# Kernel optimization log

Hardware: AMD Instinct MI355X
Metric: run time of the kernel (lower is better)

## Reference

```python
import jax, jax.numpy as jnp
import numpy as np

B, T, D, H = 2, 2048, 1024, 16
HD = D // H
FF = 4 * D
EPS = 1e-5


def rmsnorm(x, w):
    var = jnp.mean(jnp.square(x), axis=-1, keepdims=True)
    return x * jax.lax.rsqrt(var + EPS) * w


def setup_inputs() -> dict:
    key = jax.random.key(0)
    ks = jax.random.split(key, 17)
    sc = 0.02
    d = {}
    d["x"] = jax.random.normal(ks[0], (B, T, D), jnp.float32)
    d["x_token"] = jax.random.normal(ks[1], (B, T, D), jnp.float32)
    d["pos_emb"] = jax.random.normal(ks[2], (T, D), jnp.float32)
    d["lc_weight"] = jax.random.normal(ks[3], (1,), jnp.float32)
    d["Wq"] = jax.random.normal(ks[4], (D, D), jnp.float32) * sc  # per-head query weights stacked
    d["Wk"] = jax.random.normal(ks[5], (D, D), jnp.float32) * sc
    d["Wv"] = jax.random.normal(ks[6], (D, D), jnp.float32) * sc
    d["proj_w"] = jax.random.normal(ks[7], (D, D), jnp.float32) * sc
    d["proj_b"] = jnp.zeros((D,), jnp.float32)
    d["w1_w"] = jax.random.normal(ks[8], (FF, D), jnp.float32) * sc
    d["w1_b"] = jnp.zeros((FF,), jnp.float32)
    d["w2_w"] = jax.random.normal(ks[9], (D, FF), jnp.float32) * sc
    d["w2_b"] = jnp.zeros((D,), jnp.float32)
    d["w3_w"] = jax.random.normal(ks[10], (FF, D), jnp.float32) * sc
    d["w3_b"] = jnp.zeros((FF,), jnp.float32)
    d["norm1_w"] = jnp.ones((D,), jnp.float32)
    d["norm2_w"] = jnp.ones((D,), jnp.float32)
    return d


def reference(x, x_token, pos_emb, lc_weight, Wq, Wk, Wv, proj_w, proj_b,
              w1_w, w1_b, w2_w, w2_b, w3_w, w3_b, norm1_w, norm2_w):
    lc = jax.nn.sigmoid(lc_weight)  # scalar gate
    x_att = lc * x + (1.0 - lc) * x_token
    xn = rmsnorm(x_att, norm1_w)

    # q, v from normed gated input; k from raw positional embedding (faithful to source)
    q = (xn @ Wq.T).reshape(B, T, H, HD)
    k = (pos_emb @ Wk.T).reshape(T, H, HD)
    v = (xn @ Wv.T).reshape(B, T, H, HD)

    # NOTE: scale uses full model dim E (=D), not head_size, as in the source
    scores = jnp.einsum('bqhd,khd->bhqk', q, k) * (D ** -0.5)
    causal = jnp.tril(jnp.ones((T, T), bool))
    scores = jnp.where(causal, scores, -jnp.inf)
    p = jax.nn.softmax(scores, axis=-1)
    attn = jnp.einsum('bhqk,bkhd->bqhd', p, v).reshape(B, T, D)

    x = x + attn @ proj_w.T + proj_b

    xn2 = rmsnorm(x, norm2_w)
    h = jax.nn.silu(xn2 @ w1_w.T + w1_b) * (xn2 @ w3_w.T + w3_b)
    return x + h @ w2_w.T + w2_b
```

## Files before the change

kernel.cpp:

```cpp
#include <hip/hip_runtime.h>
#include <hip/hip_bf16.h>


typedef __hip_bfloat16 bf16;
typedef __attribute__((ext_vector_type(8))) short bf16x8;
typedef __attribute__((ext_vector_type(4))) float floatx4;

constexpr int cB = 2, cT = 2048, cD = 1024, cH = 16, cFF = 4096;
constexpr float cEPS = 1e-5f;
constexpr unsigned BF16_ONES = 0x3F803F80u;

__device__ __forceinline__ float b2f(bf16 x) { return __bfloat162float(x); }
__device__ __forceinline__ bf16  f2b(float x) { return __float2bfloat16(x); }
__device__ __forceinline__ unsigned short f2bu(float x) {
  bf16 t = __float2bfloat16(x);
  union { bf16 b; unsigned short u; } cv;
  cv.b = t;
  return cv.u;
}
__device__ __forceinline__ float loadR(const bf16* p)  { return b2f(*p); }
__device__ __forceinline__ float loadR(const float* p) { return *p; }

__device__ __forceinline__ void gload16(const bf16* g, unsigned short* l) {
  __builtin_amdgcn_global_load_lds(
      (const __attribute__((address_space(1))) void*)g,
      (__attribute__((address_space(3))) void*)l, 16, 0, 0);
}

__device__ __forceinline__ int xcd_remap1(int lin, int n) {
  return (lin & 7) * (n >> 3) + (lin >> 3);
}
__device__ __forceinline__ void xcd_remap(int& bx, int& by, int gx, int gy) {
  const int nwg = gx * gy;
  const int lin = by * gx + bx;
  const int nl  = xcd_remap1(lin, nwg);
  bx = nl % gx;
  by = nl / gx;
}

struct ConvArgs {
  const void* src[17];
  bf16* dst[17];
  int n[17];
  int sb[17];
};

__global__ __launch_bounds__(256) void convert_all_k(ConvArgs a) {
  const int bid = blockIdx.x;
  int seg = 0;
#pragma unroll
  for (int i = 1; i < 17; i++) seg = (bid >= a.sb[i]) ? i : seg;
  const int n = a.n[seg];
  const int i0 = (bid - a.sb[seg]) * 2048 + threadIdx.x * 8;
  if (i0 >= n) return;
  const bool isb = (((const unsigned*)a.src[15])[0] == BF16_ONES);
  const void* src = a.src[seg];
  bf16* dst = a.dst[seg];
  if (i0 + 8 <= n) {
    if (isb) {
      *(int4*)(dst + i0) = *(const int4*)((const bf16*)src + i0);
    } else {
      float4 f0 = *(const float4*)((const float*)src + i0);
      float4 f1 = *(const float4*)((const float*)src + i0 + 4);
      int4 ro;
      bf16* po = (bf16*)&ro;
      po[0] = f2b(f0.x); po[1] = f2b(f0.y); po[2] = f2b(f0.z); po[3] = f2b(f0.w);
      po[4] = f2b(f1.x); po[5] = f2b(f1.y); po[6] = f2b(f1.z); po[7] = f2b(f1.w);
      *(int4*)(dst + i0) = ro;
    }
  } else {
    for (int j = i0; j < n; j++)
      dst[j] = isb ? ((const bf16*)src)[j] : f2b(((const float*)src)[j]);
  }
}

template <int OUTK, typename ResT>
__device__ __forceinline__ void gemm_core64(
    const bf16* __restrict__ A, const bf16* __restrict__ W,
    const bf16* __restrict__ bias, const ResT* __restrict__ R,
    void* __restrict__ Cv,
    int N, int Kst, int kb, int klen, int m0, int n0,
    unsigned short* As, unsigned short* Bs)
{
  const int tid  = threadIdx.x;
  const int wave = tid >> 6;
  const int lane = tid & 63;
  const int l15  = lane & 15;
  const int quad = lane >> 4;
  const int wm   = (wave >> 1) * 64;
  const int wn   = (wave & 1) * 32;

  const int lr  = lane >> 2;
  const int lc8 = (lane & 3) * 8;
  const bf16* Ag0 = A + (size_t)(m0 + wave * 32 + lr) * Kst + kb + lc8;
  const bf16* Ag1 = Ag0 + (size_t)16 * Kst;
  const bf16* Bg0 = W + (size_t)(n0 + wave * 16 + lr) * Kst + kb + lc8;
  unsigned short* lA0 = &As[(wave * 32) * 32];
  unsigned short* lA1 = &As[(wave * 32 + 16) * 32];
  unsigned short* lB0 = &Bs[(wave * 16) * 32];

  floatx4 acc[4][2];
#pragma unroll
  for (int i = 0; i < 4; i++)
#pragma unroll
    for (int j = 0; j < 2; j++) acc[i][j] = (floatx4){0.f, 0.f, 0.f, 0.f};

  for (int k0 = 0; k0 < klen; k0 += 64) {
    gload16(Ag0 + k0, lA0);
    gload16(Ag1 + k0, lA1);
    gload16(Ag0 + k0 + 32, lA0 + 128 * 32);
    gload16(Ag1 + k0 + 32, lA1 + 128 * 32);
    gload16(Bg0 + k0, lB0);
    gload16(Bg0 + k0 + 32, lB0 + 64 * 32);
    __syncthreads();

    bf16x8 a[4][2], b[2][2];
#pragma unroll
    for (int t = 0; t < 4; t++)
#pragma unroll
      for (int kh = 0; kh < 2; kh++)
        a[t][kh] = *(const bf16x8*)&As[kh * 128 * 32 + (wm + t * 16 + l15) * 32 + quad * 8];
#pragma unroll
    for (int u = 0; u < 2; u++)
#pragma unroll
      for (int kh = 0; kh < 2; kh++)
        b[u][kh] = *(const bf16x8*)&Bs[kh * 64 * 32 + (wn + u * 16 + l15) * 32 + quad * 8];
#pragma unroll
    for (int tm = 0; tm < 4; tm++)
#pragma unroll
      for (int tn = 0; tn < 2; tn++)
#pragma unroll
        for (int kh = 0; kh < 2; kh++)
          acc[tm][tn] = __builtin_amdgcn_mfma_f32_16x16x32_bf16(a[tm][kh], b[tn][kh], acc[tm][tn], 0, 0, 0);
    __syncthreads();
  }

#pragma unroll
  for (int tm = 0; tm < 4; tm++) {
#pragma unroll
    for (int tn = 0; tn < 2; tn++) {
      const int row = m0 + wm + tm * 16 + quad * 4;
      const int col = n0 + wn + tn * 16 + l15;
      float bv = (OUTK != 3 && bias) ? b2f(bias[col]) : 0.f;
#pragma unroll
      for (int i = 0; i < 4; i++) {
        float val = acc[tm][tn][i] + bv;
        const size_t cidx = (size_t)(row + i) * N + col;
        if (OUTK == 3) {
          atomicAdd((float*)Cv + cidx, val);
        } else {
          if (R) val += loadR(&R[cidx]);
          if (OUTK == 0) ((bf16*)Cv)[cidx] = f2b(val);
          else           ((float*)Cv)[cidx] = val;
        }
      }
    }
  }
}

template <int OUTK, typename ResT>
__global__ __launch_bounds__(256) void gemm_f(
    const bf16* __restrict__ A, const bf16* __restrict__ W,
    const bf16* __restrict__ bias, const ResT* __restrict__ R,
    void* __restrict__ Cv, int N, int Kst, int kchunk, int gx, int gxy)
{
  __shared__ __align__(16) unsigned short As[2 * 128 * 32];
  __shared__ __align__(16) unsigned short Bs[2 * 64 * 32];
  const int lin = xcd_remap1(blockIdx.x, gridDim.x);
  const int kz  = lin / gxy;
  const int rem = lin % gxy;
  gemm_core64<OUTK, ResT>(A, W, bias, R, Cv, N, Kst, kz * kchunk, kchunk,
                          (rem / gx) * 128, (rem % gx) * 64, As, Bs);
}

__global__ __launch_bounds__(256) void gemm_qkv(
    const bf16* __restrict__ xn, const bf16* __restrict__ pos,
    const bf16* __restrict__ Wq, const bf16* __restrict__ Wv,
    const bf16* __restrict__ Wk,
    bf16* __restrict__ q, bf16* __restrict__ v, bf16* __restrict__ kb)
{
  __shared__ __align__(16) unsigned short As[2 * 128 * 32];
  __shared__ __align__(16) unsigned short Bs[2 * 64 * 32];
  const int lin = xcd_remap1(blockIdx.x, gridDim.x);
  int z, local;
  if (lin < 512)       { z = 0; local = lin; }
  else if (lin < 1024) { z = 1; local = lin - 512; }
  else                 { z = 2; local = lin - 1024; }
  const int gx = 16;
  const int by = local / gx, bx = local % gx;
  const bf16* A = (z == 2) ? pos : xn;
  const bf16* W = (z == 0) ? Wq : (z == 1) ? Wv : Wk;
  bf16* C = (z == 0) ? q : (z == 1) ? v : kb;
  gemm_core64<0, bf16>(A, W, nullptr, (const bf16*)nullptr, C,
                       cD, cD, 0, cD, by * 128, bx * 64, As, Bs);
}

__global__ __launch_bounds__(256, 2) void gemm_w13(
    const bf16* __restrict__ A,
    const bf16* __restrict__ W1, const bf16* __restrict__ b1,
    const bf16* __restrict__ W3, const bf16* __restrict__ b3,
    bf16* __restrict__ H, int N, int K)
{
  __shared__ __align__(16) unsigned short As[128 * 32];
  __shared__ __align__(16) unsigned short B1s[128 * 32];
  __shared__ __align__(16) unsigned short B3s[128 * 32];
  const int tid  = threadIdx.x;
  int bx = blockIdx.x, by = blockIdx.y;
  xcd_remap(bx, by, gridDim.x, gridDim.y);
  const int m0   = by * 128;
  const int n0   = bx * 128;
  const int wave = tid >> 6;
  const int lane = tid & 63;
  const int l15  = lane & 15;
  const int quad = lane >> 4;
  const int wm   = (wave >> 1) * 64;
  const int wn   = (wave & 1) * 64;

  const int lr  = lane >> 2;
  const int lc8 = (lane & 3) * 8;
  const bf16* Ag0  = A  + (size_t)(m0 + wave * 32 + lr) * K + lc8;
  const bf16* Ag1  = Ag0 + (size_t)16 * K;
  const bf16* B1g0 = W1 + (size_t)(n0 + wave * 32 + lr) * K + lc8;
  const bf16* B1g1 = B1g0 + (size_t)16 * K;
  const bf16* B3g0 = W3 + (size_t)(n0 + wave * 32 + lr) * K + lc8;
  const bf16* B3g1 = B3g0 + (size_t)16 * K;
  unsigned short* lA0 = &As[(wave * 32) * 32];
  unsigned short* lA1 = &As[(wave * 32 + 16) * 32];
  unsigned short* l10 = &B1s[(wave * 32) * 32];
  unsigned short* l11 = &B1s[(wave * 32 + 16) * 32];
  unsigned short* l30 = &B3s[(wave * 32) * 32];
  unsigned short* l31 = &B3s[(wave * 32 + 16) * 32];

  floatx4 acc1[4][4], acc3[4][4];
#pragma unroll
  for (int i = 0; i < 4; i++)
#pragma unroll
    for (int j = 0; j < 4; j++) {
      acc1[i][j] = (floatx4){0.f, 0.f, 0.f, 0.f};
      acc3[i][j] = (floatx4){0.f, 0.f, 0.f, 0.f};
    }

  for (int k0 = 0; k0 < K; k0 += 32) {
    gload16(Ag0 + k0, lA0);
    gload16(Ag1 + k0, lA1);
    gload16(B1g0 + k0, l10);
    gload16(B1g1 + k0, l11);
    gload16(B3g0 + k0, l30);
    gload16(B3g1 + k0, l31);
    __syncthreads();

    bf16x8 a[4], v1[4], v3[4];
#pragma unroll
    for (int t = 0; t < 4; t++) {
      a[t]  = *(const bf16x8*)&As[(wm + t * 16 + l15) * 32 + quad * 8];
      v1[t] = *(const bf16x8*)&B1s[(wn + t * 16 + l15) * 32 + quad * 8];
      v3[t] = *(const bf16x8*)&B3s[(wn + t * 16 + l15) * 32 + quad * 8];
    }
#pragma unroll
    for (int tm = 0; tm < 4; tm++)
#pragma unroll
      for (int tn = 0; tn < 4; tn++) {
        acc1[tm][tn] = __builtin_amdgcn_mfma_f32_16x16x32_bf16(a[tm], v1[tn], acc1[tm][tn], 0, 0, 0);
        acc3[tm][tn] = __builtin_amdgcn_mfma_f32_16x16x32_bf16(a[tm], v3[tn], acc3[tm][tn], 0, 0, 0);
      }
    __syncthreads();
  }

#pragma unroll
  for (int tm = 0; tm < 4; tm++) {
#pragma unroll
    for (int tn = 0; tn < 4; tn++) {
      const int row = m0 + wm + tm * 16 + quad * 4;
      const int col = n0 + wn + tn * 16 + l15;
      const float bv1 = b2f(b1[col]);
      const float bv3 = b2f(b3[col]);
#pragma unroll
      for (int i = 0; i < 4; i++) {
        float g = acc1[tm][tn][i] + bv1;
        float u = acc3[tm][tn][i] + bv3;
        float val = g * (1.f / (1.f + __expf(-g))) * u;
        H[(size_t)(row + i) * N + col] = f2b(val);
      }
    }
  }
}

template <bool GATE, typename InT>
__global__ __launch_bounds__(256) void rmsnorm_k(
    const InT* __restrict__ X, const bf16* __restrict__ XT,
    const bf16* __restrict__ LC, const bf16* __restrict__ Wn,
    bf16* __restrict__ O, float* __restrict__ Z)
{
  const int row = blockIdx.x;
  const int tid = threadIdx.x;
  const size_t base = (size_t)row * cD;
  const int c = tid * 4;

  if (Z) *(float4*)(Z + base + c) = (float4){0.f, 0.f, 0.f, 0.f};

  float lc = 1.f, lc1 = 0.f;
  if (GATE) {
    float g = b2f(LC[0]);
    lc = 1.f / (1.f + __expf(-g));
    lc1 = 1.f - lc;
  }

  float xv[4];
  if (sizeof(InT) == 2) {
    ushort4 u = *(const ushort4*)((const unsigned short*)X + base + c);
    const bf16* pu = (const bf16*)&u;
#pragma unroll
    for (int i = 0; i < 4; i++) xv[i] = b2f(pu[i]);
  } else {
    float4 f = *(const float4*)((const float*)X + base + c);
    xv[0] = f.x; xv[1] = f.y; xv[2] = f.z; xv[3] = f.w;
  }
  if (GATE) {
    ushort4 u = *(const ushort4*)((const unsigned short*)XT + base + c);
    const bf16* pu = (const bf16*)&u;
#pragma unroll
    for (int i = 0; i < 4; i++) xv[i] = lc * xv[i] + lc1 * b2f(pu[i]);
  }

  float ss = xv[0] * xv[0] + xv[1] * xv[1] + xv[2] * xv[2] + xv[3] * xv[3];
#pragma unroll
  for (int off = 32; off; off >>= 1) ss += __shfl_xor(ss, off, 64);

  __shared__ float red[4];
  if ((tid & 63) == 0) red[tid >> 6] = ss;
  __syncthreads();
  float tot = red[0] + red[1] + red[2] + red[3];
  float rs = rsqrtf(tot * (1.f / cD) + cEPS);

  ushort4 o;
  bf16* po = (bf16*)&o;
#pragma unroll
  for (int i = 0; i < 4; i++) po[i] = f2b(xv[i] * rs * b2f(Wn[c + i]));
  *(ushort4*)((unsigned short*)O + base + c) = o;
}

__global__ __launch_bounds__(256) void combine_k(
    const float* __restrict__ P, const float* __restrict__ X2,
    const bf16* __restrict__ bias, void* __restrict__ out,
    const unsigned* __restrict__ dbits)
{
  const bool obf = (*dbits == BF16_ONES);
  const size_t idx = ((size_t)blockIdx.x * 256 + threadIdx.x) * 4;
  float4 p = *(const float4*)(P + idx);
  float4 x = *(const float4*)(X2 + idx);
  const int col = (int)(idx & (cD - 1));
  ushort4 bu = *(const ushort4*)((const unsigned short*)bias + col);
  const bf16* bb = (const bf16*)&bu;
  float v0 = p.x + x.x + b2f(bb[0]);
  float v1 = p.y + x.y + b2f(bb[1]);
  float v2 = p.z + x.z + b2f(bb[2]);
  float v3 = p.w + x.w + b2f(bb[3]);
  if (obf) {
    ushort4 o;
    bf16* po = (bf16*)&o;
    po[0] = f2b(v0); po[1] = f2b(v1); po[2] = f2b(v2); po[3] = f2b(v3);
    *(ushort4*)((unsigned short*)out + idx) = o;
  } else {
    *(float4*)((float*)out + idx) = (float4){v0, v1, v2, v3};
  }
}

__global__ __launch_bounds__(256) void fattn_k(
    const bf16* __restrict__ Q, const bf16* __restrict__ K,
    const bf16* __restrict__ V, bf16* __restrict__ O)
{
  constexpr int LQ = 72, LK = 72, LV = 72;
  __shared__ __align__(16) unsigned short Qs[64 * LQ];
  __shared__ __align__(16) unsigned short Ks[64 * LK];
  __shared__ __align__(16) unsigned short Vs[64 * LV];

  const int tid  = threadIdx.x;
  const int wave = tid >> 6;
  const int lane = tid & 63;
  const int l15  = lane & 15;
  const int quad = lane >> 4;
  const int blk  = blockIdx.x;
  const int qt   = 31 - (blk & 31);
  const int h    = (blk >> 5) & 15;
  const int b    = blk >> 9;
  const int q0   = qt * 64;

  const bf16* Qb = Q + ((size_t)b * cT) * cD + h * 64;
  const bf16* Kb = K + h * 64;
  const bf16* Vb = V + ((size_t)b * cT) * cD + h * 64;

  {
    const int qr = tid >> 2, qc = (tid & 3) * 16;
    const bf16* gq = Qb + (size_t)(q0 + qr) * cD + qc;
    *(int4*)&Qs[qr * LQ + qc]     = *(const int4*)(gq);
    *(int4*)&Qs[qr * LQ + qc + 8] = *(const int4*)(gq + 8);
  }
  __syncthreads();

  const int qw = wave * 16;
  bf16x8 qa[2];
#pragma unroll
  for (int dc = 0; dc < 2; dc++)
    qa[dc] = *(const bf16x8*)&Qs[(qw + l15) * LQ + dc * 32 + quad * 8];

  float l_p[4] = {0.f, 0.f, 0.f, 0.f};
  floatx4 oacc[4];
#pragma unroll
  for (int dt = 0; dt < 4; dt++) oacc[dt] = (floatx4){0.f, 0.f, 0.f, 0.f};

  const int ktiles = qt + 1;
  unsigned short* Pw = &Qs[qw * LQ];

  const int kr = tid >> 2, kc = (tid & 3) * 16;
  int4 kpre0, kpre1;
  unsigned short vpre[16];
  {
    const bf16* g = Kb + (size_t)kr * cD + kc;
    kpre0 = *(const int4*)g;
    kpre1 = *(const int4*)(g + 8);
    const unsigned short* gv = (const unsigned short*)(Vb + (size_t)(wave * 16) * cD + lane);
#pragma unroll
    for (int j = 0; j < 16; j++) vpre[j] = gv[(size_t)j * cD];
  }

  for (int it = 0; it < ktiles; ++it) {
    const int k0 = it * 64;
    __syncthreads();
    *(int4*)&Ks[kr * LK + kc]     = kpre0;
    *(int4*)&Ks[kr * LK + kc + 8] = kpre1;
    {
      union { unsigned short us[8]; int4 v4; } pk0, pk1;
#pragma unroll
      for (int j = 0; j < 8; j++) { pk0.us[j] = vpre[j]; pk1.us[j] = vpre[8 + j]; }
      *(int4*)&Vs[lane * LV + wave * 16]     = pk0.v4;
      *(int4*)&Vs[lane * LV + wave * 16 + 8] = pk1.v4;
    }
    __syncthreads();

    if (it + 1 < ktiles) {
      const bf16* g = Kb + (size_t)(k0 + 64 + kr) * cD + kc;
      kpre0 = *(const int4*)g;
      kpre1 = *(const int4*)(g + 8);
      const unsigned short* gv = (const unsigned short*)(Vb + (size_t)(k0 + 64 + wave * 16) * cD + lane);
#pragma unroll
      for (int j = 0; j < 16; j++) vpre[j] = gv[(size_t)j * cD];
    }

    floatx4 s[4];
#pragma unroll
    for (int st = 0; st < 4; st++) {
      bf16x8 kb0 = *(const bf16x8*)&Ks[(st * 16 + l15) * LK + quad * 8];
      bf16x8 kb1 = *(const bf16x8*)&Ks[(st * 16 + l15) * LK + 32 + quad * 8];
      s[st] = (floatx4){0.f, 0.f, 0.f, 0.f};
      s[st] = __builtin_amdgcn_mfma_f32_16x16x32_bf16(qa[0], kb0, s[st], 0, 0, 0);
      s[st] = __builtin_amdgcn_mfma_f32_16x16x32_bf16(qa[1], kb1, s[st], 0, 0, 0);
    }
    float p[4][4];
#pragma unroll
    for (int i = 0; i < 4; i++) {
      const int qrow = q0 + qw + quad * 4 + i;
#pragma unroll
      for (int st = 0; st < 4; st++) {
        const int kp = k0 + st * 16 + l15;
        float pv = (kp > qrow) ? 0.f : __expf(s[st][i] * 0.03125f);
        p[st][i] = pv;
        l_p[i] += pv;
      }
    }
#pragma unroll
    for (int st = 0; st < 4; st++)
#pragma unroll
      for (int i = 0; i < 4; i++)
        Pw[(quad * 4 + i) * LQ + st * 16 + l15] = f2bu(p[st][i]);
    bf16x8 pa[2];
#pragma unroll
    for (int pc = 0; pc < 2; pc++)
      pa[pc] = *(const bf16x8*)&Pw[l15 * LQ + pc * 32 + quad * 8];
#pragma unroll
    for (int dt = 0; dt < 4; dt++) {
      bf16x8 vb0 = *(const bf16x8*)&Vs[(dt * 16 + l15) * LV + quad * 8];
      bf16x8 vb1 = *(const bf16x8*)&Vs[(dt * 16 + l15) * LV + 32 + quad * 8];
      oacc[dt] = __builtin_amdgcn_mfma_f32_16x16x32_bf16(pa[0], vb0, oacc[dt], 0, 0, 0);
      oacc[dt] = __builtin_amdgcn_mfma_f32_16x16x32_bf16(pa[1], vb1, oacc[dt], 0, 0, 0);
    }
  }

  float rl[4];
#pragma unroll
  for (int i = 0; i < 4; i++) {
    float li = l_p[i];
#pragma unroll
    for (int off = 1; off < 16; off <<= 1) li += __shfl_xor(li, off, 64);
    rl[i] = 1.f / li;
  }
  const size_t obase = ((size_t)b * cT + q0 + qw) * cD + h * 64;
#pragma unroll
  for (int dt = 0; dt < 4; dt++)
#pragma unroll
    for (int i = 0; i < 4; i++)
      O[obase + (size_t)(quad * 4 + i) * cD + dt * 16 + l15] = f2b(oacc[dt][i] * rl[i]);
}

extern "C" void kernel_launch(void* const* d_in, const int* in_sizes, int n_in,
                              void* d_out, int out_size, void* d_ws, size_t ws_size,
                              hipStream_t stream) {
  char* ws = (char*)d_ws;
  const size_t MB = 1u << 20;
  const int BT = cB * cT;

  bf16* cxt  = (bf16*)(ws + 0);
  bf16* cpos = (bf16*)(ws + 8 * MB);
  bf16* q    = (bf16*)(ws + 12 * MB);
  bf16* kbuf = (bf16*)(ws + 20 * MB);
  bf16* v    = (bf16*)(ws + 24 * MB);
  bf16* h    = (bf16*)(ws + 0);
  size_t off = 32 * MB;
  auto alloc = [&](size_t bytes) -> char* {
    char* p = ws + off;
    off = (off + bytes + 255) & ~(size_t)255;
    return p;
  };
  bf16*  cx  = (bf16*)alloc((size_t)BT * cD * 2);
  bf16*  xn  = (bf16*)alloc((size_t)BT * cD * 2);
  float* x2  = (float*)alloc((size_t)BT * cD * 4);
  bf16*  xn2 = (bf16*)alloc((size_t)BT * cD * 2);
  float* part = (float*)(ws + 32 * MB);
  bf16* cin[17];
  cin[0] = cx; cin[1] = cxt; cin[2] = cpos;
  for (int i = 3; i < 17; i++) cin[i] = (bf16*)alloc((size_t)in_sizes[i] * 2);

  const unsigned* dbits = (const unsigned*)d_in[15];
  dim3 blk(256);

  ConvArgs ca;
  int nblk = 0;
  for (int i = 0; i < 17; i++) {
    ca.src[i] = d_in[i];
    ca.dst[i] = cin[i];
    ca.n[i] = in_sizes[i];
    ca.sb[i] = nblk;
    nblk += (in_sizes[i] + 2047) / 2048;
  }
  convert_all_k<<<nblk, blk, 0, stream>>>(ca);

  const bf16 *clc = cin[3], *cWq = cin[4], *cWk = cin[5], *cWv = cin[6];
  const bf16 *cprojw = cin[7], *cprojb = cin[8];
  const bf16 *cw1w = cin[9], *cw1b = cin[10], *cw2w = cin[11], *cw2b = cin[12];
  const bf16 *cw3w = cin[13], *cw3b = cin[14], *cn1 = cin[15], *cn2 = cin[16];

  rmsnorm_k<true, bf16><<<BT, blk, 0, stream>>>(cx, cxt, clc, cn1, xn, nullptr);
  gemm_qkv<<<1280, blk, 0, stream>>>(xn, cpos, cWq, cWv, cWk, q, v, kbuf);
  bf16* attn = xn;
  fattn_k<<<cB * cH * (cT / 64), blk, 0, stream>>>(q, kbuf, v, attn);
  gemm_f<1, bf16><<<512, blk, 0, stream>>>(
      attn, cprojw, cprojb, cx, x2, cD, cD, cD, 16, 512);
  rmsnorm_k<false, float><<<BT, blk, 0, stream>>>(
      x2, (const bf16*)nullptr, (const bf16*)nullptr, cn2, xn2, part);
  gemm_w13<<<dim3(cFF / 128, BT / 128), blk, 0, stream>>>(
      xn2, cw1w, cw1b, cw3w, cw3b, h, cFF, cD);
  gemm_f<3, float><<<1024, blk, 0, stream>>>(
      h, cw2w, nullptr, (const float*)nullptr, part, cD, cFF, 2048, 16, 512);
  combine_k<<<BT, blk, 0, stream>>>(part, x2, cw2b, d_out, dbits);
  (void)n_in; (void)out_size; (void)ws_size;
}
```

Measured before the change: 466.9 us.

## Retile fused W1/W3 GEMM to 128x64 tiles with K=64 steps and 1D grid

The gate/up GEMM now uses 128x64 output tiles instead of 128x128 and processes 64 K elements per barrier pair instead of 32. It launches a 1D grid of 2048 blocks with an XCD-aware remap. The smaller per-wave accumulator set (16 floatx4 instead of 32) lowers register pressure, so the min-blocks launch bound is dropped. The goal is better occupancy, more blocks to spread across CUs, and half as many syncthreads per K. The cost is less reuse of the A tile per block, so A is read from memory more often.

```diff
diff --git a/kernel.cpp b/kernel.cpp
--- a/kernel.cpp
+++ b/kernel.cpp
@@ -195,81 +195,89 @@
                        cD, cD, 0, cD, by * 128, bx * 64, As, Bs);
 }
 
-__global__ __launch_bounds__(256, 2) void gemm_w13(
+__global__ __launch_bounds__(256) void gemm_w13(
     const bf16* __restrict__ A,
     const bf16* __restrict__ W1, const bf16* __restrict__ b1,
     const bf16* __restrict__ W3, const bf16* __restrict__ b3,
     bf16* __restrict__ H, int N, int K)
 {
-  __shared__ __align__(16) unsigned short As[128 * 32];
-  __shared__ __align__(16) unsigned short B1s[128 * 32];
-  __shared__ __align__(16) unsigned short B3s[128 * 32];
+  __shared__ __align__(16) unsigned short As[2 * 128 * 32];
+  __shared__ __align__(16) unsigned short B1s[2 * 64 * 32];
+  __shared__ __align__(16) unsigned short B3s[2 * 64 * 32];
+  const int lin = xcd_remap1(blockIdx.x, gridDim.x);
+  const int by  = lin & 31;
+  const int bx  = lin >> 5;
+  const int m0  = by * 128;
+  const int n0  = bx * 64;
+
   const int tid  = threadIdx.x;
-  int bx = blockIdx.x, by = blockIdx.y;
-  xcd_remap(bx, by, gridDim.x, gridDim.y);
-  const int m0   = by * 128;
-  const int n0   = bx * 128;
   const int wave = tid >> 6;
   const int lane = tid & 63;
   const int l15  = lane & 15;
   const int quad = lane >> 4;
   const int wm   = (wave >> 1) * 64;
-  const int wn   = (wave & 1) * 64;
+  const int wn   = (wave & 1) * 32;
 
   const int lr  = lane >> 2;
   const int lc8 = (lane & 3) * 8;
   const bf16* Ag0  = A  + (size_t)(m0 + wave * 32 + lr) * K + lc8;
   const bf16* Ag1  = Ag0 + (size_t)16 * K;
-  const bf16* B1g0 = W1 + (size_t)(n0 + wave * 32 + lr) * K + lc8;
-  const bf16* B1g1 = B1g0 + (size_t)16 * K;
-  const bf16* B3g0 = W3 + (size_t)(n0 + wave * 32 + lr) * K + lc8;
-  const bf16* B3g1 = B3g0 + (size_t)16 * K;
+  const bf16* B1g0 = W1 + (size_t)(n0 + wave * 16 + lr) * K + lc8;
+  const bf16* B3g0 = W3 + (size_t)(n0 + wave * 16 + lr) * K + lc8;
   unsigned short* lA0 = &As[(wave * 32) * 32];
   unsigned short* lA1 = &As[(wave * 32 + 16) * 32];
-  unsigned short* l10 = &B1s[(wave * 32) * 32];
-  unsigned short* l11 = &B1s[(wave * 32 + 16) * 32];
-  unsigned short* l30 = &B3s[(wave * 32) * 32];
-  unsigned short* l31 = &B3s[(wave * 32 + 16) * 32];
-
-  floatx4 acc1[4][4], acc3[4][4];
+  unsigned short* l1B = &B1s[(wave * 16) * 32];
+  unsigned short* l3B = &B3s[(wave * 16) * 32];
+
+  floatx4 acc1[4][2], acc3[4][2];
 #pragma unroll
   for (int i = 0; i < 4; i++)
 #pragma unroll
-    for (int j = 0; j < 4; j++) {
+    for (int j = 0; j < 2; j++) {
       acc1[i][j] = (floatx4){0.f, 0.f, 0.f, 0.f};
       acc3[i][j] = (floatx4){0.f, 0.f, 0.f, 0.f};
     }
 
-  for (int k0 = 0; k0 < K; k0 += 32) {
+  for (int k0 = 0; k0 < K; k0 += 64) {
     gload16(Ag0 + k0, lA0);
     gload16(Ag1 + k0, lA1);
-    gload16(B1g0 + k0, l10);
-    gload16(B1g1 + k0, l11);
-    gload16(B3g0 + k0, l30);
-    gload16(B3g1 + k0, l31);
+    gload16(Ag0 + k0 + 32, lA0 + 128 * 32);
+    gload16(Ag1 + k0 + 32, lA1 + 128 * 32);
+    gload16(B1g0 + k0, l1B);
+    gload16(B1g0 + k0 + 32, l1B + 64 * 32);
+    gload16(B3g0 + k0, l3B);
+    gload16(B3g0 + k0 + 32, l3B + 64 * 32);
     __syncthreads();
 
-    bf16x8 a[4], v1[4], v3[4];
-#pragma unroll
-    for (int t = 0; t < 4; t++) {
-      a[t]  = *(const bf16x8*)&As[(wm + t * 16 + l15) * 32 + quad * 8];
-      v1[t] = *(const bf16x8*)&B1s[(wn + t * 16 + l15) * 32 + quad * 8];
-      v3[t] = *(const bf16x8*)&B3s[(wn + t * 16 + l15) * 32 + quad * 8];
-    }
+    bf16x8 a[4][2], v1[2][2], v3[2][2];
+#pragma unroll
+    for (int t = 0; t < 4; t++)
+#pragma unroll
+      for (int kh = 0; kh < 2; kh++)
+        a[t][kh] = *(const bf16x8*)&As[kh * 128 * 32 + (wm + t * 16 + l15) * 32 + quad * 8];
+#pragma unroll
+    for (int u = 0; u < 2; u++)
+#pragma unroll
+      for (int kh = 0; kh < 2; kh++) {
+        v1[u][kh] = *(const bf16x8*)&B1s[kh * 64 * 32 + (wn + u * 16 + l15) * 32 + quad * 8];
+        v3[u][kh] = *(const bf16x8*)&B3s[kh * 64 * 32 + (wn + u * 16 + l15) * 32 + quad * 8];
+      }
 #pragma unroll
     for (int tm = 0; tm < 4; tm++)
 #pragma unroll
-      for (int tn = 0; tn < 4; tn++) {
-        acc1[tm][tn] = __builtin_amdgcn_mfma_f32_16x16x32_bf16(a[tm], v1[tn], acc1[tm][tn], 0, 0, 0);
-        acc3[tm][tn] = __builtin_amdgcn_mfma_f32_16x16x32_bf16(a[tm], v3[tn], acc3[tm][tn], 0, 0, 0);
-      }
+      for (int tn = 0; tn < 2; tn++)
+#pragma unroll
+        for (int kh = 0; kh < 2; kh++) {
+          acc1[tm][tn] = __builtin_amdgcn_mfma_f32_16x16x32_bf16(a[tm][kh], v1[tn][kh], acc1[tm][tn], 0, 0, 0);
+          acc3[tm][tn] = __builtin_amdgcn_mfma_f32_16x16x32_bf16(a[tm][kh], v3[tn][kh], acc3[tm][tn], 0, 0, 0);
+        }
     __syncthreads();
   }
 
 #pragma unroll
   for (int tm = 0; tm < 4; tm++) {
 #pragma unroll
-    for (int tn = 0; tn < 4; tn++) {
+    for (int tn = 0; tn < 2; tn++) {
       const int row = m0 + wm + tm * 16 + quad * 4;
       const int col = n0 + wn + tn * 16 + l15;
       const float bv1 = b2f(b1[col]);
@@ -556,7 +564,7 @@
       attn, cprojw, cprojb, cx, x2, cD, cD, cD, 16, 512);
   rmsnorm_k<false, float><<<BT, blk, 0, stream>>>(
       x2, (const bf16*)nullptr, (const bf16*)nullptr, cn2, xn2, part);
-  gemm_w13<<<dim3(cFF / 128, BT / 128), blk, 0, stream>>>(
+  gemm_w13<<<2048, blk, 0, stream>>>(
       xn2, cw1w, cw1b, cw3w, cw3b, h, cFF, cD);
   gemm_f<3, float><<<1024, blk, 0, stream>>>(
       h, cw2w, nullptr, (const float*)nullptr, part, cD, cFF, 2048, 16, 512);
```

After: 471.3 us. Within noise of the previous version (+0.9%).
